# Kernel optimization log

Hardware: AMD Instinct MI355X
Metric: run time of the kernel (lower is better)

Reference implementation:

```python
import jax, jax.numpy as jnp
import numpy as np
from jax import lax

# Dims from LSTMTagger class constants
B, S, LP = 1024, 128, 14       # sentences, words/sentence, padded chars/word
K, CE, WE, Lf = 3, 6, 10, 4    # char window, char emb, word emb, cnn filters
H, V, A, T = 6, 50000, 100, 135  # lstm hidden, vocab, alphabet, tagset
D = WE + Lf                     # lstm input dim = 14
LW = LP - K + 1                 # conv windows per word = 12


def setup_inputs() -> dict:
    key = jax.random.key(0)
    ks = jax.random.split(key, 14)
    n = lambda k, shp: jax.random.normal(k, shp, dtype=jnp.float32) * 0.1
    inp = {
        "word_idx": jax.random.randint(ks[0], (B, S), 0, V, dtype=jnp.int32),
        "char_idx": jax.random.randint(ks[1], (B, S, LP), 0, A, dtype=jnp.int32),
        "word_emb": n(ks[2], (V, WE)),
        "char_emb": n(ks[3], (A, CE)),
        "Wc": n(ks[4], (Lf, K * CE)),   # Conv1d(1, l, K*CE) weight, squeezed
        "bc": n(ks[5], (Lf,)),
        "Wih_f": n(ks[6], (4 * H, D)),
        "Whh_f": n(ks[7], (4 * H, H)),
        "b_f": n(ks[8], (4 * H,)),      # b_ih + b_hh fused (equivalent)
        "Wih_b": n(ks[9], (4 * H, D)),
        "Whh_b": n(ks[10], (4 * H, H)),
        "b_b": n(ks[11], (4 * H,)),
        "Wt": n(ks[12], (T, 2 * H)),
        "bt": n(ks[13], (T,)),
    }
    return inp


def _lstm_scan(xs, Wih, Whh, b):
    # xs: [S, B, D] -> hs: [S, B, H]; torch gate order i, f, g, o
    h0 = jnp.zeros((xs.shape[1], H), xs.dtype)

    def step(carry, xt):
        h, c = carry
        g = xt @ Wih.T + h @ Whh.T + b
        i, f, gg, o = jnp.split(g, 4, axis=-1)
        c = jax.nn.sigmoid(f) * c + jax.nn.sigmoid(i) * jnp.tanh(gg)
        h = jax.nn.sigmoid(o) * jnp.tanh(c)
        return (h, c), h

    _, hs = lax.scan(step, (h0, h0), xs)
    return hs


def reference(word_emb, char_emb, Wc, bc, Wih_f, Whh_f, b_f,
              Wih_b, Whh_b, b_b, Wt, bt, word_idx, char_idx):
    # per-word char CNN: sliding K-char windows, flatten, linear, max-pool
    ce = char_emb[char_idx]                              # [B,S,LP,CE]
    windows = jnp.concatenate([ce[:, :, i:i + LW] for i in range(K)], axis=-1)  # [B,S,LW,K*CE]
    phi = jnp.einsum('bswk,lk->bswl', windows, Wc) + bc  # [B,S,LW,Lf]
    char_repr = phi.max(axis=2)                          # [B,S,Lf]

    we = word_emb[word_idx]                              # [B,S,WE]
    x = jnp.concatenate([we, char_repr], axis=-1)        # [B,S,D]

    xs = x.transpose(1, 0, 2)                            # [S,B,D]
    hf = _lstm_scan(xs, Wih_f, Whh_f, b_f)               # forward direction
    hb = _lstm_scan(xs[::-1], Wih_b, Whh_b, b_b)[::-1]   # backward direction
    out = jnp.concatenate([hf, hb], axis=-1).transpose(1, 0, 2)  # [B,S,2H]

    tag_space = out @ Wt.T + bt                          # [B,S,T]
    return jax.nn.log_softmax(tag_space, axis=-1)
```

## Files before the change

### kernel.cpp

```cpp
#include <hip/hip_runtime.h>

#define B_   1024
#define S_   128
#define LP_  14
#define K_   3
#define CE_  6
#define WE_  10
#define LF_  4
#define H_   6
#define D_   14
#define T_   135
#define LW_  12
#define V_   50000
#define A_   100

static __device__ __forceinline__ float sigm(float x) {
    float e = __expf(-fabsf(x));
    float r = __frcp_rn(1.0f + e);
    return (x >= 0.f) ? r : e * r;
}
static __device__ __forceinline__ float tanh_(float x) {
    float e = __expf(-2.0f * fabsf(x));
    float r = (1.0f - e) * __frcp_rn(1.0f + e);
    return (x >= 0.f) ? r : -r;
}

__global__ __launch_bounds__(256) void k_el(
    const int* __restrict__ word_idx, const int* __restrict__ char_idx,
    const float* __restrict__ word_emb, const float* __restrict__ char_emb,
    const float* __restrict__ Wc, const float* __restrict__ bc,
    const float* __restrict__ Wih_f, const float* __restrict__ Whh_f, const float* __restrict__ b_f,
    const float* __restrict__ Wih_b, const float* __restrict__ Whh_b, const float* __restrict__ b_b,
    float* __restrict__ hbuf)
{
    __shared__ float s_x[512][16];
    __shared__ float s_h[4][S_][12];
    __shared__ float s_ce[A_ * CE_];
    __shared__ float s_wc[LF_ * K_ * CE_];
    __shared__ float s_bc[LF_];

    int t = threadIdx.x;
    for (int e = t; e < A_ * CE_; e += 256) s_ce[e] = char_emb[e];
    if (t < LF_ * K_ * CE_) s_wc[t] = Wc[t];
    if (t < LF_) s_bc[t] = bc[t];
    __syncthreads();

    int Wbase = blockIdx.x * 512;
    #pragma unroll
    for (int rep = 0; rep < 2; ++rep) {
        int wl = t + rep * 256;
        int w  = Wbase + wl;
        const int2* ci2 = (const int2*)(char_idx + (size_t)w * LP_);
        int idxs[LP_];
        #pragma unroll
        for (int p = 0; p < 7; ++p) {
            int2 v = ci2[p];
            idxs[2 * p] = v.x; idxs[2 * p + 1] = v.y;
        }
        float ce[LP_][CE_];
        #pragma unroll
        for (int p = 0; p < LP_; ++p) {
            int idx = idxs[p];
            idx = idx < 0 ? 0 : (idx >= A_ ? A_ - 1 : idx);
            #pragma unroll
            for (int c = 0; c < CE_; ++c) ce[p][c] = s_ce[idx * CE_ + c];
        }
        float xr[16];
        #pragma unroll
        for (int l = 0; l < LF_; ++l) {
            float acc[LW_];
            float bl = s_bc[l];
            #pragma unroll
            for (int q = 0; q < LW_; ++q) acc[q] = bl;
            #pragma unroll
            for (int kk = 0; kk < K_; ++kk) {
                #pragma unroll
                for (int c = 0; c < CE_; ++c) {
                    float wv_ = s_wc[l * (K_ * CE_) + kk * CE_ + c];
                    #pragma unroll
                    for (int q = 0; q < LW_; ++q) acc[q] = fmaf(ce[q + kk][c], wv_, acc[q]);
                }
            }
            float m = acc[0];
            #pragma unroll
            for (int q = 1; q < LW_; ++q) m = fmaxf(m, acc[q]);
            xr[WE_ + l] = m;
        }
        int wi = word_idx[w];
        wi = wi < 0 ? 0 : (wi >= V_ ? V_ - 1 : wi);
        const float2* wep = (const float2*)(word_emb + (size_t)wi * WE_);
        #pragma unroll
        for (int c = 0; c < WE_ / 2; ++c) {
            float2 v = wep[c];
            xr[2 * c] = v.x; xr[2 * c + 1] = v.y;
        }
        xr[14] = 0.f; xr[15] = 0.f;
        float4* xp = (float4*)&s_x[wl][0];
        xp[0] = make_float4(xr[0], xr[1], xr[2], xr[3]);
        xp[1] = make_float4(xr[4], xr[5], xr[6], xr[7]);
        xp[2] = make_float4(xr[8], xr[9], xr[10], xr[11]);
        xp[3] = make_float4(xr[12], xr[13], xr[14], xr[15]);
    }
    __syncthreads();

    int wv   = t >> 6;
    int lane = t & 63;
    int dir  = lane >> 5;
    int l    = lane & 31;
    bool act = (l < 24);
    int u = act ? (l % 6) : 0;
    int j = act ? (l / 6) : 0;
    int base = dir << 5;
    bool isg = (j == 2);

    {
        const float* Wih = dir ? Wih_b : Wih_f;
        const float* Whh = dir ? Whh_b : Whh_f;
        const float* bi  = dir ? b_b  : b_f;
        int r = j * H_ + u;
        float wih[D_], whh[H_], bias;
        #pragma unroll
        for (int k = 0; k < D_; ++k) wih[k] = Wih[r * D_ + k];
        #pragma unroll
        for (int k = 0; k < H_; ++k) whh[k] = Whh[r * H_ + k];
        bias = bi[r];

        float h[H_];
        #pragma unroll
        for (int k = 0; k < H_; ++k) h[k] = 0.f;
        float c = 0.f;

        float ax = bias;
        {
            const float* xp = &s_x[wv * S_ + (dir ? S_ - 1 : 0)][0];
            #pragma unroll
            for (int k = 0; k < D_; ++k) ax = fmaf(wih[k], xp[k], ax);
        }
        for (int s = 0; s < S_; ++s) {
            int se = dir ? (S_ - 1 - s) : s;
            float a = ax;
            #pragma unroll
            for (int k = 0; k < H_; ++k) a = fmaf(whh[k], h[k], a);
            float xx = isg ? (a + a) : a;
            float sg = sigm(xx);
            float ac = isg ? fmaf(2.f, sg, -1.f) : sg;
            float vi = __shfl(ac, base + u,      64);
            float vf = __shfl(ac, base + u + 6,  64);
            float vg = __shfl(ac, base + u + 12, 64);
            float vo = __shfl(ac, base + u + 18, 64);
            c = fmaf(vf, c, vi * vg);
            float hu = vo * tanh_(c);
            if (act && j == 0) s_h[wv][se][dir * H_ + u] = hu;
            #pragma unroll
            for (int k = 0; k < H_; ++k) h[k] = __shfl(hu, base + k, 64);
            if (s + 1 < S_) {
                const float* xp = &s_x[wv * S_ + (dir ? S_ - 2 - s : s + 1)][0];
                float t2 = bias;
                #pragma unroll
                for (int k = 0; k < D_; ++k) t2 = fmaf(wih[k], xp[k], t2);
                ax = t2;
            }
        }
    }
    __syncthreads();

    {
        float4* dst = (float4*)(hbuf + (size_t)blockIdx.x * 4 * S_ * 12);
        const float4* src = (const float4*)&s_h[0][0][0];
        #pragma unroll
        for (int i = 0; i < 6; ++i) dst[t + 256 * i] = src[t + 256 * i];
    }
}

__global__ __launch_bounds__(256) void k_p(
    const float* __restrict__ hbuf,
    const float* __restrict__ Wt, const float* __restrict__ bt,
    float* __restrict__ out)
{
    __shared__ float s_hb[64 * 12];
    int t = threadIdx.x;
    int ib = blockIdx.x * 64;
    {
        const float4* src = (const float4*)(hbuf + (size_t)ib * 12);
        float4* dst = (float4*)s_hb;
        if (t < 192) dst[t] = src[t];
    }
    __syncthreads();

    int lane = t & 63, wv = t >> 6;
    bool has2 = (lane < T_ - 128);
    int t2c = has2 ? (lane + 128) : (T_ - 1);

    float wA[12], wB[12], wC[12];
    #pragma unroll
    for (int jj = 0; jj < 12; ++jj) {
        wA[jj] = Wt[lane * 12 + jj];
        wB[jj] = Wt[(lane + 64) * 12 + jj];
        wC[jj] = Wt[t2c * 12 + jj];
    }
    float bA = bt[lane], bB = bt[lane + 64], bC = bt[t2c];

    int it0 = wv * 16;
    #pragma unroll 4
    for (int k = 0; k < 16; ++k) {
        int it = it0 + k;
        const float4* h4 = (const float4*)(s_hb + it * 12);
        float4 a0 = h4[0], a1 = h4[1], a2 = h4[2];
        float hv[12] = {a0.x, a0.y, a0.z, a0.w, a1.x, a1.y, a1.z, a1.w, a2.x, a2.y, a2.z, a2.w};
        float y0 = bA, y1 = bB, y2 = bC;
        #pragma unroll
        for (int jj = 0; jj < 12; ++jj) {
            y0 = fmaf(hv[jj], wA[jj], y0);
            y1 = fmaf(hv[jj], wB[jj], y1);
            y2 = fmaf(hv[jj], wC[jj], y2);
        }
        float ss = __expf(y0) + __expf(y1) + (has2 ? __expf(y2) : 0.0f);
        #pragma unroll
        for (int mk = 1; mk < 64; mk <<= 1) ss += __shfl_xor(ss, mk, 64);
        float ls = __logf(ss);
        float* op = out + (size_t)(ib + it) * T_;
        op[lane]      = y0 - ls;
        op[lane + 64] = y1 - ls;
        if (has2) op[lane + 128] = y2 - ls;
    }
}

extern "C" void kernel_launch(void* const* d_in, const int* in_sizes, int n_in,
                              void* d_out, int out_size, void* d_ws, size_t ws_size,
                              hipStream_t stream)
{
    const int* word_idx = (const int*)d_in[0];
    const int* char_idx = (const int*)d_in[1];
    const float* word_emb = (const float*)d_in[2];
    const float* char_emb = (const float*)d_in[3];
    const float* Wc    = (const float*)d_in[4];
    const float* bc    = (const float*)d_in[5];
    const float* Wih_f = (const float*)d_in[6];
    const float* Whh_f = (const float*)d_in[7];
    const float* b_f   = (const float*)d_in[8];
    const float* Wih_b = (const float*)d_in[9];
    const float* Whh_b = (const float*)d_in[10];
    const float* b_b   = (const float*)d_in[11];
    const float* Wt    = (const float*)d_in[12];
    const float* bt    = (const float*)d_in[13];

    float* hbuf = (float*)d_ws;

    k_el<<<B_ / 4, 256, 0, stream>>>(word_idx, char_idx, word_emb, char_emb, Wc, bc,
                                     Wih_f, Whh_f, b_f, Wih_b, Whh_b, b_b, hbuf);
    k_p<<<(B_ * S_) / 64, 256, 0, stream>>>(hbuf, Wt, bt, (float*)d_out);
}
```

Measured before the change: 164.3 us.

## Split LSTM into input-projection kernel and DPP-based recurrent scan kernel

The fused embed+LSTM kernel becomes two kernels. The first computes the char CNN, the word embedding and the full input-to-gate projection for both directions, and writes the gate pre-activations to a global workspace laid out by timestep. The second runs the recurrence with 4 lanes per sentence, one per gate, each lane handling all 6 hidden units, exchanging gates via DPP quad broadcasts instead of ds shuffles, and prefetching gate inputs 3 steps ahead. This shortens the serial per-step dependency chain but adds a large global round trip for the gate buffer and an extra launch.

```diff
diff --git a/kernel.cpp b/kernel.cpp
--- a/kernel.cpp
+++ b/kernel.cpp
@@ -14,42 +14,43 @@
 #define V_   50000
 #define A_   100
 
-static __device__ __forceinline__ float sigm(float x) {
-    float e = __expf(-fabsf(x));
-    float r = __frcp_rn(1.0f + e);
-    return (x >= 0.f) ? r : e * r;
-}
-static __device__ __forceinline__ float tanh_(float x) {
-    float e = __expf(-2.0f * fabsf(x));
-    float r = (1.0f - e) * __frcp_rn(1.0f + e);
-    return (x >= 0.f) ? r : -r;
-}
-
-__global__ __launch_bounds__(256) void k_el(
+#define GSTR (2 * 1024 * 24)
+#define DSTR (1024 * 24)
+
+
+template <int SRC>
+static __device__ __forceinline__ float qb(float v) {
+    constexpr int ctrl = SRC | (SRC << 2) | (SRC << 4) | (SRC << 6);
+    return __int_as_float(__builtin_amdgcn_update_dpp(
+        0, __float_as_int(v), ctrl, 0xF, 0xF, true));
+}
+
+__global__ __launch_bounds__(256) void k_eg(
     const int* __restrict__ word_idx, const int* __restrict__ char_idx,
     const float* __restrict__ word_emb, const float* __restrict__ char_emb,
     const float* __restrict__ Wc, const float* __restrict__ bc,
-    const float* __restrict__ Wih_f, const float* __restrict__ Whh_f, const float* __restrict__ b_f,
-    const float* __restrict__ Wih_b, const float* __restrict__ Whh_b, const float* __restrict__ b_b,
-    float* __restrict__ hbuf)
-{
-    __shared__ float s_x[512][16];
-    __shared__ float s_h[4][S_][12];
+    const float* __restrict__ Wih_f, const float* __restrict__ b_f,
+    const float* __restrict__ Wih_b, const float* __restrict__ b_b,
+    float* __restrict__ Gx)
+{
     __shared__ float s_ce[A_ * CE_];
     __shared__ float s_wc[LF_ * K_ * CE_];
     __shared__ float s_bc[LF_];
+    __shared__ float s_wih[2][24 * D_];
+    __shared__ float s_b[2][24];
 
     int t = threadIdx.x;
     for (int e = t; e < A_ * CE_; e += 256) s_ce[e] = char_emb[e];
     if (t < LF_ * K_ * CE_) s_wc[t] = Wc[t];
     if (t < LF_) s_bc[t] = bc[t];
+    for (int e = t; e < 24 * D_; e += 256) { s_wih[0][e] = Wih_f[e]; s_wih[1][e] = Wih_b[e]; }
+    if (t < 24) { s_b[0][t] = b_f[t]; s_b[1][t] = b_b[t]; }
     __syncthreads();
 
     int Wbase = blockIdx.x * 512;
     #pragma unroll
     for (int rep = 0; rep < 2; ++rep) {
-        int wl = t + rep * 256;
-        int w  = Wbase + wl;
+        int w = Wbase + t + rep * 256;
         const int2* ci2 = (const int2*)(char_idx + (size_t)w * LP_);
         int idxs[LP_];
         #pragma unroll
@@ -65,7 +66,7 @@
             #pragma unroll
             for (int c = 0; c < CE_; ++c) ce[p][c] = s_ce[idx * CE_ + c];
         }
-        float xr[16];
+        float xr[D_];
         #pragma unroll
         for (int l = 0; l < LF_; ++l) {
             float acc[LW_];
@@ -94,81 +95,106 @@
             float2 v = wep[c];
             xr[2 * c] = v.x; xr[2 * c + 1] = v.y;
         }
-        xr[14] = 0.f; xr[15] = 0.f;
-        float4* xp = (float4*)&s_x[wl][0];
-        xp[0] = make_float4(xr[0], xr[1], xr[2], xr[3]);
-        xp[1] = make_float4(xr[4], xr[5], xr[6], xr[7]);
-        xp[2] = make_float4(xr[8], xr[9], xr[10], xr[11]);
-        xp[3] = make_float4(xr[12], xr[13], xr[14], xr[15]);
-    }
-    __syncthreads();
-
-    int wv   = t >> 6;
-    int lane = t & 63;
-    int dir  = lane >> 5;
-    int l    = lane & 31;
-    bool act = (l < 24);
-    int u = act ? (l % 6) : 0;
-    int j = act ? (l / 6) : 0;
-    int base = dir << 5;
-    bool isg = (j == 2);
-
-    {
-        const float* Wih = dir ? Wih_b : Wih_f;
-        const float* Whh = dir ? Whh_b : Whh_f;
-        const float* bi  = dir ? b_b  : b_f;
-        int r = j * H_ + u;
-        float wih[D_], whh[H_], bias;
-        #pragma unroll
-        for (int k = 0; k < D_; ++k) wih[k] = Wih[r * D_ + k];
-        #pragma unroll
-        for (int k = 0; k < H_; ++k) whh[k] = Whh[r * H_ + k];
-        bias = bi[r];
-
-        float h[H_];
-        #pragma unroll
-        for (int k = 0; k < H_; ++k) h[k] = 0.f;
-        float c = 0.f;
-
-        float ax = bias;
-        {
-            const float* xp = &s_x[wv * S_ + (dir ? S_ - 1 : 0)][0];
-            #pragma unroll
-            for (int k = 0; k < D_; ++k) ax = fmaf(wih[k], xp[k], ax);
-        }
-        for (int s = 0; s < S_; ++s) {
+
+        int b = w >> 7, s = w & (S_ - 1);
+        float* gout = Gx + (size_t)s * GSTR + (size_t)b * 24;
+        #pragma unroll
+        for (int dir = 0; dir < 2; ++dir) {
+            float gx[24];
+            #pragma unroll
+            for (int r = 0; r < 24; ++r) {
+                float a = s_b[dir][r];
+                const float* wr = &s_wih[dir][r * D_];
+                #pragma unroll
+                for (int k = 0; k < D_; ++k) a = fmaf(wr[k], xr[k], a);
+                gx[r] = a;
+            }
+            float4* gp = (float4*)(gout + dir * DSTR);
+            #pragma unroll
+            for (int r4 = 0; r4 < 6; ++r4)
+                gp[r4] = make_float4(gx[4 * r4], gx[4 * r4 + 1], gx[4 * r4 + 2], gx[4 * r4 + 3]);
+        }
+    }
+}
+
+__global__ __launch_bounds__(64) void k_scan(
+    const float* __restrict__ Gx,
+    const float* __restrict__ Whh_f, const float* __restrict__ Whh_b,
+    float* __restrict__ hbuf)
+{
+    int wg   = blockIdx.x;
+    int dir  = wg & 1;
+    int b0   = (wg >> 1) << 4;
+    int lane = threadIdx.x & 63;
+    int ch   = lane >> 2;
+    int q    = lane & 3;
+    int b    = b0 + ch;
+
+    const float* Whh = dir ? Whh_b : Whh_f;
+    float whh[H_][H_];
+    #pragma unroll
+    for (int u = 0; u < H_; ++u)
+        #pragma unroll
+        for (int k = 0; k < H_; ++k) whh[u][k] = Whh[(q * H_ + u) * H_ + k];
+
+    float kIn = (q == 2) ? -2.f : -1.f;
+    float kM  = (q == 2) ?  2.f :  1.f;
+    float kB  = (q == 2) ? -1.f :  0.f;
+
+    const float* gb = Gx + (size_t)dir * DSTR + (size_t)b * 24 + q * H_;
+
+    float buf[4][H_];
+    auto loadg = [&](int slot, int tt) {
+        int se = dir ? (S_ - 1 - tt) : tt;
+        se = se < 0 ? 0 : (se > S_ - 1 ? S_ - 1 : se);
+        const float2* p = (const float2*)(gb + (size_t)se * GSTR);
+        float2 v0 = p[0], v1 = p[1], v2 = p[2];
+        buf[slot][0] = v0.x; buf[slot][1] = v0.y; buf[slot][2] = v1.x;
+        buf[slot][3] = v1.y; buf[slot][4] = v2.x; buf[slot][5] = v2.y;
+    };
+    loadg(0, 0); loadg(1, 1); loadg(2, 2);
+
+    float h[H_], c[H_];
+    #pragma unroll
+    for (int u = 0; u < H_; ++u) { h[u] = 0.f; c[u] = 0.f; }
+
+    float* hb = hbuf + (size_t)b * S_ * 12 + dir * H_;
+
+    for (int sb = 0; sb < S_; sb += 4) {
+        #pragma unroll
+        for (int k = 0; k < 4; ++k) {
+            int s  = sb + k;
             int se = dir ? (S_ - 1 - s) : s;
-            float a = ax;
-            #pragma unroll
-            for (int k = 0; k < H_; ++k) a = fmaf(whh[k], h[k], a);
-            float xx = isg ? (a + a) : a;
-            float sg = sigm(xx);
-            float ac = isg ? fmaf(2.f, sg, -1.f) : sg;
-            float vi = __shfl(ac, base + u,      64);
-            float vf = __shfl(ac, base + u + 6,  64);
-            float vg = __shfl(ac, base + u + 12, 64);
-            float vo = __shfl(ac, base + u + 18, 64);
-            c = fmaf(vf, c, vi * vg);
-            float hu = vo * tanh_(c);
-            if (act && j == 0) s_h[wv][se][dir * H_ + u] = hu;
-            #pragma unroll
-            for (int k = 0; k < H_; ++k) h[k] = __shfl(hu, base + k, 64);
-            if (s + 1 < S_) {
-                const float* xp = &s_x[wv * S_ + (dir ? S_ - 2 - s : s + 1)][0];
-                float t2 = bias;
+            float g[H_];
+            #pragma unroll
+            for (int u = 0; u < H_; ++u) {
+                float a = buf[k][u];
                 #pragma unroll
-                for (int k = 0; k < D_; ++k) t2 = fmaf(wih[k], xp[k], t2);
-                ax = t2;
-            }
-        }
-    }
-    __syncthreads();
-
-    {
-        float4* dst = (float4*)(hbuf + (size_t)blockIdx.x * 4 * S_ * 12);
-        const float4* src = (const float4*)&s_h[0][0][0];
-        #pragma unroll
-        for (int i = 0; i < 6; ++i) dst[t + 256 * i] = src[t + 256 * i];
+                for (int k2 = 0; k2 < H_; ++k2) a = fmaf(whh[u][k2], h[k2], a);
+                g[u] = a;
+            }
+            #pragma unroll
+            for (int u = 0; u < H_; ++u) {
+                float e = __expf(kIn * g[u]);
+                float r = __frcp_rn(1.f + e);
+                g[u] = fmaf(kM, r, kB);
+            }
+            #pragma unroll
+            for (int u = 0; u < H_; ++u) {
+                float gi = qb<0>(g[u]);
+                float gf = qb<1>(g[u]);
+                float gg = qb<2>(g[u]);
+                float go = qb<3>(g[u]);
+                c[u] = fmaf(gf, c[u], gi * gg);
+                float e  = __expf(-2.f * c[u]);
+                float th = fmaf(2.f, __frcp_rn(1.f + e), -1.f);
+                h[u] = go * th;
+            }
+            float s0 = (q == 0) ? h[0] : ((q == 1) ? h[1] : ((q == 2) ? h[2] : h[3]));
+            hb[(size_t)se * 12 + q] = s0;
+            if (q < 2) hb[(size_t)se * 12 + 4 + q] = (q == 0) ? h[4] : h[5];
+            loadg((k + 3) & 3, s + 3);
+        }
     }
 }
 
@@ -245,8 +271,10 @@
     const float* bt    = (const float*)d_in[13];
 
     float* hbuf = (float*)d_ws;
-
-    k_el<<<B_ / 4, 256, 0, stream>>>(word_idx, char_idx, word_emb, char_emb, Wc, bc,
-                                     Wih_f, Whh_f, b_f, Wih_b, Whh_b, b_b, hbuf);
+    float* Gx   = hbuf + (size_t)B_ * S_ * 12;
+
+    k_eg<<<(B_ * S_) / 512, 256, 0, stream>>>(word_idx, char_idx, word_emb, char_emb,
+                                              Wc, bc, Wih_f, b_f, Wih_b, b_b, Gx);
+    k_scan<<<(B_ / 16) * 2, 64, 0, stream>>>(Gx, Whh_f, Whh_b, hbuf);
     k_p<<<(B_ * S_) / 64, 256, 0, stream>>>(hbuf, Wt, bt, (float*)d_out);
 }
```

Measured after the change: 248.9 us. +51.5%, slower.
